# Kernel tuning notes

Measured on AMD Instinct MI355X. Metric: run time of the kernel, lower is better.

## Reference

```python
import jax, jax.numpy as jnp
import numpy as np

H, HKV, D, BS, NSEL, WIN = 32, 8, 64, 64, 16, 512
N_REP = H // HKV


def precompute_freqs(dim, max_seq_len, theta=10000.0):
    inv = 1.0 / theta ** (np.arange(0, dim, 2, dtype=np.float32) / dim)
    t = np.arange(max_seq_len, dtype=np.float32)
    return jnp.asarray(np.outer(t, inv))  # (S, dim//2)


def apply_rope(x, freqs):
    # x: (B, T, H, D)
    T = x.shape[1]
    xr = x.reshape(x.shape[:-1] + (-1, 2))
    cos = jnp.cos(freqs[:T])[None, :, None, :]
    sin = jnp.sin(freqs[:T])[None, :, None, :]
    x0, x1 = xr[..., 0], xr[..., 1]
    out = jnp.stack([x0 * cos - x1 * sin, x0 * sin + x1 * cos], axis=-1)
    return out.reshape(x.shape)


def setup_inputs() -> dict:
    key = jax.random.key(0)
    ks = jax.random.split(key, 9)
    d_model = 2048
    s = lambda fan_in: 1.0 / np.sqrt(fan_in)
    return {
        "x": jax.random.normal(ks[0], (1, 2048, d_model), jnp.float32),
        "W_q": jax.random.normal(ks[1], (d_model, H * D), jnp.float32) * s(d_model),
        "W_k": jax.random.normal(ks[2], (d_model, HKV * D), jnp.float32) * s(d_model),
        "W_v": jax.random.normal(ks[3], (d_model, HKV * D), jnp.float32) * s(d_model),
        "W_o": jax.random.normal(ks[4], (H * D, d_model), jnp.float32) * s(H * D),
        "W_ck": jax.random.normal(ks[5], (BS * D, D), jnp.float32) * s(BS * D),
        "W_cv": jax.random.normal(ks[6], (BS * D, D), jnp.float32) * s(BS * D),
        "W_imp": jax.random.normal(ks[7], (D, 1), jnp.float32) * s(D),
        "W_gate": jax.random.normal(ks[8], (d_model, 3), jnp.float32) * s(d_model),
    }


def reference(x, W_q, W_k, W_v, W_o, W_ck, W_cv, W_imp, W_gate):
    B, T, _ = x.shape
    S = T  # no kv_cache
    scale = 1.0 / np.sqrt(D)
    freqs = precompute_freqs(D, T)

    q = apply_rope((x @ W_q).reshape(B, T, H, D), freqs)
    k = apply_rope((x @ W_k).reshape(B, T, HKV, D), freqs)
    v = (x @ W_v).reshape(B, T, HKV, D)
    q = q.transpose(0, 2, 1, 3)  # (B,H,T,D)
    k = k.transpose(0, 2, 1, 3)  # (B,HKV,S,D)
    v = v.transpose(0, 2, 1, 3)

    # --- compressed-block branch ---
    nb = S // BS
    kb = k[:, :, : nb * BS].reshape(B, HKV, nb, BS * D)
    vb = v[:, :, : nb * BS].reshape(B, HKV, nb, BS * D)
    kc = jnp.repeat(kb @ W_ck, N_REP, axis=1)  # (B,H,nb,D)
    vc = jnp.repeat(vb @ W_cv, N_REP, axis=1)
    a_c = jax.nn.softmax(jnp.einsum('bhtd,bhnd->bhtn', q, kc) * scale, axis=-1)
    out_c = jnp.einsum('bhtn,bhnd->bhtd', a_c, vc)

    # GQA expansion shared by select / sliding branches
    kx = jnp.repeat(k, N_REP, axis=1)
    vx = jnp.repeat(v, N_REP, axis=1)

    # --- 'selected' branch (reference computes top-k indices but discards them;
    # attention is full dense unmasked softmax, faithfully reproduced) ---
    k_mean = k[:, :, : nb * BS].reshape(B, HKV, nb, BS, D).mean(axis=3)
    scores = (k_mean @ W_imp)[..., 0]
    _top = jax.lax.top_k(scores, NSEL)  # dead code in original; kept for faithfulness
    a_s = jax.nn.softmax(jnp.einsum('bhtd,bhsd->bhts', q, kx) * scale, axis=-1)
    out_s = jnp.einsum('bhts,bhsd->bhtd', a_s, vx)

    # --- sliding-window branch (dense scores + mask, as in original) ---
    logits = jnp.einsum('bhtd,bhsd->bhts', q, kx) * scale
    i = jnp.arange(T)[:, None]
    j = jnp.arange(S)[None, :]
    allowed = (j <= S - T + i) & (j >= S - T + i - WIN + 1)
    logits = jnp.where(allowed[None, None], logits, -jnp.inf)
    a_w = jnp.nan_to_num(jax.nn.softmax(logits, axis=-1))
    out_w = jnp.einsum('bhts,bhsd->bhtd', a_w, vx)

    # --- gated combine ---
    gates = jax.nn.softmax(x @ W_gate, axis=-1)  # (B,T,3)
    stacked = jnp.stack(
        [out_c.transpose(0, 2, 1, 3), out_s.transpose(0, 2, 1, 3), out_w.transpose(0, 2, 1, 3)],
        axis=3,
    )  # (B,T,H,3,D)
    out = (stacked * gates[:, :, None, :, None]).sum(axis=3).reshape(B, T, H * D)
    return out @ W_o
```

## Files before the change

kernel.cpp:

```cpp
#include <hip/hip_runtime.h>
#include <cmath>

typedef unsigned short u16;
typedef unsigned int u32;
typedef __attribute__((ext_vector_type(8))) __bf16 bf16x8;
typedef __attribute__((ext_vector_type(8))) u16 u16x8;
typedef __attribute__((ext_vector_type(4))) float f32x4;
typedef __attribute__((ext_vector_type(4))) u16 u16x4;

#define MFMA16(acc, a, b) (acc) = __builtin_amdgcn_mfma_f32_16x16x32_bf16((a), (b), (acc), 0, 0, 0)

__device__ __forceinline__ u16 f2bf(float x) {
  union { float f; u32 u; } c; c.f = x;
  u32 r = (c.u + 0x7FFFu + ((c.u >> 16) & 1u)) >> 16;
  return (u16)r;
}
__device__ __forceinline__ float bf2f(u16 b) {
  union { u32 u; float f; } c; c.u = ((u32)b) << 16;
  return c.f;
}
__device__ __forceinline__ float rowmax16(float v) {
#pragma unroll
  for (int m = 1; m < 16; m <<= 1) v = fmaxf(v, __shfl_xor(v, m));
  return v;
}
__device__ __forceinline__ float rowsum16(float v) {
#pragma unroll
  for (int m = 1; m < 16; m <<= 1) v += __shfl_xor(v, m);
  return v;
}
__device__ __forceinline__ void gload16(const u16* g, u16* l) {
  __builtin_amdgcn_global_load_lds(
      (const __attribute__((address_space(1))) void*)(g),
      (__attribute__((address_space(3))) void*)(l), 16, 0, 0);
}
__device__ __forceinline__ float exp2_asm(float x) {
  float r;
  asm("v_exp_f32 %0, %1\n\ts_nop 0" : "=v"(r) : "v"(x));
  return r;
}
__device__ __forceinline__ u32 cvtpk(float a, float b) {
  u32 r;
  asm("v_cvt_pk_bf16_f32 %0, %1, %2" : "=v"(r) : "v"(a), "v"(b));
  return r;
}
__device__ __forceinline__ u16x8 bc_u(bf16x8 v) { union { bf16x8 b; u16x8 u; } c; c.b = v; return c.u; }
__device__ __forceinline__ bf16x8 bc_b(u16x8 v) { union { u16x8 u; bf16x8 b; } c; c.u = v; return c.b; }
__device__ __forceinline__ bf16x8 pack8(f32x4 a, f32x4 b) {
  union { u32 w[4]; bf16x8 v; } c;
  c.w[0] = cvtpk(a[0], a[1]);
  c.w[1] = cvtpk(a[2], a[3]);
  c.w[2] = cvtpk(b[0], b[1]);
  c.w[3] = cvtpk(b[2], b[3]);
  return c.v;
}

__global__ void freqs_kernel(float* __restrict__ ct, float* __restrict__ st) {
  int idx = blockIdx.x * 256 + threadIdx.x;
  int t = idx >> 5, i = idx & 31;
  float inv = 1.0f / powf(10000.0f, (float)i / 32.0f);
  float a = (float)t * inv;
  float sv, cv;
  sincosf(a, &sv, &cv);
  ct[idx] = cv;
  st[idx] = sv;
}

__global__ void cvt_x_kernel(const float* __restrict__ in, u16* __restrict__ out) {
  int idx = (blockIdx.x * 256 + threadIdx.x) * 4;
  f32x4 v = *(const f32x4*)(in + idx);
  u16x4 o;
  o[0] = f2bf(v[0]); o[1] = f2bf(v[1]); o[2] = f2bf(v[2]); o[3] = f2bf(v[3]);
  *(u16x4*)(out + idx) = o;
}

__global__ __launch_bounds__(256) void trcvt_kernel(const float* __restrict__ W,
                                                    u16* __restrict__ Wt, int K, int N) {
  __shared__ u16 t_lds[64][65];
  int ntx = N >> 6;
  int kt = (blockIdx.x / ntx) * 64, nt = (blockIdx.x % ntx) * 64;
  int tx = threadIdx.x & 63, ty4 = threadIdx.x >> 6;
#pragma unroll 4
  for (int yy = 0; yy < 16; ++yy) {
    int k = kt + ty4 * 16 + yy;
    t_lds[ty4 * 16 + yy][tx] = f2bf(W[(size_t)k * N + nt + tx]);
  }
  __syncthreads();
#pragma unroll 4
  for (int yy = 0; yy < 16; ++yy) {
    int n = nt + ty4 * 16 + yy;
    Wt[(size_t)n * K + kt + tx] = t_lds[tx][ty4 * 16 + yy];
  }
}

__global__ __launch_bounds__(256) void gemm_bt_kernel(const u16* __restrict__ A,
                                                      const u16* __restrict__ Bt,
                                                      float* __restrict__ C,
                                                      int M, int N, int K) {
  __shared__ __align__(16) u16 As[128 * 64];
  __shared__ __align__(16) u16 Bs[128 * 64];
  const int tid = threadIdx.x;
  const int lane = tid & 63;
  const int w = tid >> 6;
  const int lr = lane & 15;
  const int lg = lane >> 4;
  const int lk8 = lg * 8;
  const int gx = gridDim.x;
  const int nwg = gx * gridDim.y;
  const int flat = blockIdx.y * gx + blockIdx.x;
  const int qq = nwg >> 3;
  const int swz = (flat & 7) * qq + (flat >> 3);
  const int brow = (swz % gx) * 128;
  const int bcol = (swz / gx) * 128;
  const int wr = (w >> 1) * 64;
  const int wc = (w & 1) * 64;

  const f32x4 zero4 = {0.f, 0.f, 0.f, 0.f};
  f32x4 acc[4][4];
#pragma unroll
  for (int m = 0; m < 4; ++m)
#pragma unroll
    for (int n = 0; n < 4; ++n) acc[m][n] = zero4;

  const int srow = tid >> 3;
  const int scol = (tid & 7) * 8;
  const u16* Ab = A + (size_t)(brow + srow) * K + scol;
  const u16* Bb = Bt + (size_t)(bcol + srow) * K + scol;

  for (int k0 = 0; k0 < K; k0 += 64) {
    __syncthreads();
#pragma unroll
    for (int it = 0; it < 4; ++it) {
      gload16(Ab + (size_t)it * 32 * K + k0, &As[tid * 8 + it * 2048]);
      gload16(Bb + (size_t)it * 32 * K + k0, &Bs[tid * 8 + it * 2048]);
    }
    __syncthreads();
#pragma unroll
    for (int kk = 0; kk < 2; ++kk) {
      bf16x8 af[4], bv[4];
#pragma unroll
      for (int m = 0; m < 4; ++m)
        af[m] = *(const bf16x8*)&As[(wr + m * 16 + lr) * 64 + kk * 32 + lk8];
#pragma unroll
      for (int n = 0; n < 4; ++n)
        bv[n] = *(const bf16x8*)&Bs[(wc + n * 16 + lr) * 64 + kk * 32 + lk8];
#pragma unroll
      for (int m = 0; m < 4; ++m)
#pragma unroll
        for (int n = 0; n < 4; ++n) MFMA16(acc[m][n], af[m], bv[n]);
    }
  }
#pragma unroll
  for (int m = 0; m < 4; ++m) {
#pragma unroll
    for (int rr = 0; rr < 4; ++rr) {
      int row = brow + wr + m * 16 + lg * 4 + rr;
#pragma unroll
      for (int n = 0; n < 4; ++n)
        C[(size_t)row * N + bcol + wc + n * 16 + lr] = acc[m][n][rr];
    }
  }
}

__global__ void rope_q_kernel(const float* __restrict__ qkv, const float* __restrict__ ct,
                              const float* __restrict__ st, u16* __restrict__ qb) {
  int idx = blockIdx.x * 256 + threadIdx.x;
  int i = idx & 31, hh = (idx >> 5) & 31, t = idx >> 10;
  float x0 = qkv[(size_t)t * 3072 + hh * 64 + 2 * i];
  float x1 = qkv[(size_t)t * 3072 + hh * 64 + 2 * i + 1];
  float c = ct[t * 32 + i], s = st[t * 32 + i];
  size_t o = ((size_t)hh * 2048 + t) * 64 + 2 * i;
  qb[o] = f2bf((x0 * c - x1 * s) * 0.125f);
  qb[o + 1] = f2bf((x0 * s + x1 * c) * 0.125f);
}
__global__ void rope_k_kernel(const float* __restrict__ qkv, const float* __restrict__ ct,
                              const float* __restrict__ st, u16* __restrict__ kb) {
  int idx = blockIdx.x * 256 + threadIdx.x;
  int i = idx & 31, hh = (idx >> 5) & 7, t = idx >> 8;
  float x0 = qkv[(size_t)t * 3072 + 2048 + hh * 64 + 2 * i];
  float x1 = qkv[(size_t)t * 3072 + 2048 + hh * 64 + 2 * i + 1];
  float c = ct[t * 32 + i], s = st[t * 32 + i];
  size_t o = ((size_t)hh * 2048 + t) * 64 + 2 * i;
  kb[o] = f2bf(x0 * c - x1 * s);
  kb[o + 1] = f2bf(x0 * s + x1 * c);
}
__global__ __launch_bounds__(256) void vtrans_kernel(const float* __restrict__ qkv,
                                                     u16* __restrict__ vbr,
                                                     u16* __restrict__ vb2) {
  __shared__ u16 tl[64][72];
  int hk = blockIdx.y, t0 = blockIdx.x * 64;
  int tx = threadIdx.x & 63, ty = threadIdx.x >> 6;
#pragma unroll 4
  for (int yy = 0; yy < 16; ++yy) {
    int row = ty * 16 + yy;
    u16 b = f2bf(qkv[(size_t)(t0 + row) * 3072 + 2560 + hk * 64 + tx]);
    tl[row][tx] = b;
    vbr[((size_t)hk * 2048 + t0 + row) * 64 + tx] = b;
  }
  __syncthreads();
  u16* dst = vb2 + (size_t)hk * 64 * 2048 + t0;
#pragma unroll 4
  for (int yy = 0; yy < 16; ++yy)
    dst[(size_t)(ty * 16 + yy) * 2048 + tx] = tl[tx][ty * 16 + yy];
}

__global__ __launch_bounds__(256) void gates_kernel(const float* __restrict__ x,
                                                    const float* __restrict__ Wg,
                                                    float* __restrict__ g) {
  int t = blockIdx.x * 4 + (threadIdx.x >> 6);
  int lane = threadIdx.x & 63;
  const float* xr = x + (size_t)t * 2048;
  float a0 = 0, a1 = 0, a2 = 0;
  for (int d = lane; d < 2048; d += 64) {
    float xv = xr[d];
    a0 = fmaf(xv, Wg[d * 3 + 0], a0);
    a1 = fmaf(xv, Wg[d * 3 + 1], a1);
    a2 = fmaf(xv, Wg[d * 3 + 2], a2);
  }
#pragma unroll
  for (int msk = 1; msk < 64; msk <<= 1) {
    a0 += __shfl_xor(a0, msk);
    a1 += __shfl_xor(a1, msk);
    a2 += __shfl_xor(a2, msk);
  }
  if (lane == 0) {
    float m = fmaxf(a0, fmaxf(a1, a2));
    float e0 = __expf(a0 - m), e1 = __expf(a1 - m), e2 = __expf(a2 - m);
    float inv = 1.f / (e0 + e1 + e2);
    g[t * 3 + 0] = e0 * inv; g[t * 3 + 1] = e1 * inv; g[t * 3 + 2] = e2 * inv;
  }
}

__global__ __launch_bounds__(256) void cgemm_kernel(const u16* __restrict__ kB,
                                                    const u16* __restrict__ vbr,
                                                    const float* __restrict__ Wck,
                                                    const float* __restrict__ Wcv,
                                                    float* __restrict__ kc,
                                                    float* __restrict__ vc) {
  __shared__ float red[4][64];
  int b = blockIdx.x;
  bool isv = b >= 256;
  int blk = b & 255;
  const u16* src = (isv ? vbr : kB) + (size_t)blk * 4096;
  const float* W = isv ? Wcv : Wck;
  float* out = (isv ? vc : kc) + (size_t)blk * 64;
  int lane = threadIdx.x & 63, w = threadIdx.x >> 6;
  int base = w * 1024;
  float acc0 = 0.f, acc1 = 0.f;
  for (int i = 0; i < 1024; i += 8) {
    u16x8 s8 = *(const u16x8*)(src + base + i);
#pragma unroll
    for (int j = 0; j < 8; j += 2) {
      acc0 = fmaf(bf2f(s8[j]), W[(size_t)(base + i + j) * 64 + lane], acc0);
      acc1 = fmaf(bf2f(s8[j + 1]), W[(size_t)(base + i + j + 1) * 64 + lane], acc1);
    }
  }
  red[w][lane] = acc0 + acc1;
  __syncthreads();
  if (w == 0)
    out[lane] = red[0][lane] + red[1][lane] + red[2][lane] + red[3][lane];
}

__global__ __launch_bounds__(256) void attn_kernel(
    const u16* __restrict__ qb, const u16* __restrict__ kb, const u16* __restrict__ vb2,
    const float* __restrict__ kcf, const float* __restrict__ vcf,
    const float* __restrict__ gf, u16* __restrict__ comb) {
  __shared__ __align__(16) u16 k_lds[2][64 * 64];
  __shared__ __align__(16) u16 vt_lds[2][64 * 64];
  __shared__ __align__(16) u16 p_lds[4][16 * 64];

  const int tid = threadIdx.x;
  const int lane = tid & 63;
  const int w = tid >> 6;
  const int lr = lane & 15;
  const int lg = lane >> 4;
  const int lk8 = lg * 8;
  const int flat = blockIdx.y * gridDim.x + blockIdx.x;
  const int swz = (flat & 7) * 128 + (flat >> 3);
  const int h = swz >> 5;
  const int t0 = (swz & 31) * 64;
  const int hk = h >> 2;
  const int tw = t0 + w * 16;
  const f32x4 zero4 = {0.f, 0.f, 0.f, 0.f};
  const float LOG2E = 1.44269504f;
  const float THR = 11.5416f;

  bf16x8 qf0, qf1;
  {
    const u16* qrow = qb + ((size_t)h * 2048 + (tw + lr)) * 64;
    qf0 = *(const bf16x8*)(qrow + lk8);
    qf1 = *(const bf16x8*)(qrow + 32 + lk8);
  }

  const int lin1 = 256 + tid;
  const int row0 = tid >> 3, sl0 = (tid & 7) ^ (row0 & 7);
  const int row1 = lin1 >> 3, sl1 = (lin1 & 7) ^ (row1 & 7);
  const u16* kS0 = kb + ((size_t)hk * 2048 + row0) * 64 + sl0 * 8;
  const u16* kS1 = kb + ((size_t)hk * 2048 + row1) * 64 + sl1 * 8;
  const u16* vS0 = vb2 + ((size_t)hk * 64 + row0) * 2048 + sl0 * 8;
  const u16* vS1 = vb2 + ((size_t)hk * 64 + row1) * 2048 + sl1 * 8;

  const int sA = ((0 + lg) ^ (lr & 7)) * 8;
  const int sB = ((4 + lg) ^ (lr & 7)) * 8;

  f32x4 acc_s[4], acc_w[4];
#pragma unroll
  for (int n = 0; n < 4; ++n) { acc_s[n] = zero4; acc_w[n] = zero4; }
  float m2[4], lsr[4], lwr[4];
#pragma unroll
  for (int r = 0; r < 4; ++r) { m2[r] = -1e30f; lsr[r] = 0.f; lwr[r] = 0.f; }

#define STAGE(cc)                                                      \
  {                                                                    \
    const int b_ = (cc) & 1;                                           \
    gload16(kS0 + (size_t)(cc) * 4096, &k_lds[b_][tid * 8]);           \
    gload16(kS1 + (size_t)(cc) * 4096, &k_lds[b_][2048 + tid * 8]);    \
    gload16(vS0 + (cc) * 64, &vt_lds[b_][tid * 8]);                    \
    gload16(vS1 + (cc) * 64, &vt_lds[b_][2048 + tid * 8]);             \
  }

  STAGE(0);
  __syncthreads();

#pragma unroll 1
  for (int c = 0; c < 32; ++c) {
    const int s0 = c * 64;
    const u16* kbuf = k_lds[c & 1];
    const u16* vbuf = vt_lds[c & 1];
    if (c < 31) STAGE(c + 1);

    f32x4 sc[4];
    __builtin_amdgcn_s_setprio(1);
#pragma unroll
    for (int cb = 0; cb < 4; ++cb) {
      f32x4 z = zero4;
      const int rb = (cb * 16 + lr) * 64;
      bf16x8 b0 = *(const bf16x8*)&kbuf[rb + sA];
      bf16x8 b1 = *(const bf16x8*)&kbuf[rb + sB];
      MFMA16(z, qf0, b0);
      MFMA16(z, qf1, b1);
      sc[cb] = z;
    }
    __builtin_amdgcn_s_setprio(0);

    const bool winAct = (s0 <= tw + 15) && (s0 + 63 >= tw - 511);
    const int dbase = tw + lg * 4 - s0 - lr;

    float mxl[4];
#pragma unroll
    for (int r = 0; r < 4; ++r)
      mxl[r] = fmaxf(fmaxf(sc[0][r], sc[1][r]), fmaxf(sc[2][r], sc[3][r]));
    float dmax = fmaxf(fmaxf(fmaf(mxl[0], LOG2E, -m2[0]), fmaf(mxl[1], LOG2E, -m2[1])),
                       fmaxf(fmaf(mxl[2], LOG2E, -m2[2]), fmaf(mxl[3], LOG2E, -m2[3])));
    if (__any(dmax > THR)) {
#pragma unroll
      for (int r = 0; r < 4; ++r) {
        float mnew = fmaxf(m2[r], rowmax16(mxl[r]) * LOG2E);
        float corr = exp2_asm(m2[r] - mnew);
        m2[r] = mnew;
        lsr[r] *= corr;
        lwr[r] *= corr;
#pragma unroll
        for (int n = 0; n < 4; ++n) { acc_s[n][r] *= corr; acc_w[n][r] *= corr; }
      }
    }

#pragma unroll
    for (int r = 0; r < 4; ++r) {
      float pv0 = exp2_asm(fmaf(sc[0][r], LOG2E, -m2[r]));
      float pv1 = exp2_asm(fmaf(sc[1][r], LOG2E, -m2[r]));
      float pv2 = exp2_asm(fmaf(sc[2][r], LOG2E, -m2[r]));
      float pv3 = exp2_asm(fmaf(sc[3][r], LOG2E, -m2[r]));
      lsr[r] += (pv0 + pv1) + (pv2 + pv3);
      if (winAct) {
        int d0 = dbase + r;
        float s = 0.f;
        s += ((u32)d0 < 512u) ? pv0 : 0.f;
        s += ((u32)(d0 - 16) < 512u) ? pv1 : 0.f;
        s += ((u32)(d0 - 32) < 512u) ? pv2 : 0.f;
        s += ((u32)(d0 - 48) < 512u) ? pv3 : 0.f;
        lwr[r] += s;
      }
      u32 pk01 = cvtpk(pv0, pv1), pk23 = cvtpk(pv2, pv3);
      const int prow = lg * 4 + r;
      const int pb = prow * 64 + (lr & 7);
      const int rh = prow & 7;
      const int shi = lr >> 3;
      u16* pl = p_lds[w];
      pl[pb + ((0 + shi) ^ rh) * 8] = (u16)pk01;
      pl[pb + ((2 + shi) ^ rh) * 8] = (u16)(pk01 >> 16);
      pl[pb + ((4 + shi) ^ rh) * 8] = (u16)pk23;
      pl[pb + ((6 + shi) ^ rh) * 8] = (u16)(pk23 >> 16);
    }
    asm volatile("s_waitcnt lgkmcnt(0)" ::: "memory");
    bf16x8 ap0 = *(const bf16x8*)&p_lds[w][lr * 64 + sA];
    bf16x8 ap1 = *(const bf16x8*)&p_lds[w][lr * 64 + sB];

    bf16x8 aw0 = ap0, aw1 = ap1;
    if (winAct) {
      const int base0 = (tw + lr) - (s0 + lk8);
      u16x8 a0 = bc_u(ap0), a1 = bc_u(ap1);
      u16x8 z0, z1;
#pragma unroll
      for (int j = 0; j < 8; ++j) {
        z0[j] = ((u32)(base0 - j) < 512u) ? a0[j] : (u16)0;
        z1[j] = ((u32)(base0 - 32 - j) < 512u) ? a1[j] : (u16)0;
      }
      aw0 = bc_b(z0);
      aw1 = bc_b(z1);
    }

    __builtin_amdgcn_s_setprio(1);
#pragma unroll
    for (int n = 0; n < 4; ++n) {
      const int rb = (n * 16 + lr) * 64;
      bf16x8 bv0 = *(const bf16x8*)&vbuf[rb + sA];
      bf16x8 bv1 = *(const bf16x8*)&vbuf[rb + sB];
      MFMA16(acc_s[n], ap0, bv0);
      MFMA16(acc_s[n], ap1, bv1);
      if (winAct) {
        MFMA16(acc_w[n], aw0, bv0);
        MFMA16(acc_w[n], aw1, bv1);
      }
    }
    __builtin_amdgcn_s_setprio(0);

    __syncthreads();
  }
#undef STAGE

  f32x4 accc[4];
  float lcv[4];
  {
    f32x4 sc0 = zero4, sc1 = zero4;
#pragma unroll
    for (int kk = 0; kk < 2; ++kk) {
      const float* kr0 = kcf + ((size_t)hk * 32 + 0 * 16 + lr) * 64 + kk * 32 + lk8;
      const float* kr1 = kcf + ((size_t)hk * 32 + 1 * 16 + lr) * 64 + kk * 32 + lk8;
      bf16x8 b0 = pack8(*(const f32x4*)kr0, *(const f32x4*)(kr0 + 4));
      bf16x8 b1 = pack8(*(const f32x4*)kr1, *(const f32x4*)(kr1 + 4));
      bf16x8 qk = kk ? qf1 : qf0;
      MFMA16(sc0, qk, b0);
      MFMA16(sc1, qk, b1);
    }
#pragma unroll
    for (int r = 0; r < 4; ++r) {
      float a = sc0[r], b = sc1[r];
      float m = rowmax16(fmaxf(a, b));
      float p0 = __expf(a - m), p1 = __expf(b - m);
      lcv[r] = rowsum16(p0 + p1);
      u32 pk = cvtpk(p0, p1);
      const int prow = lg * 4 + r;
      const int pb = prow * 64 + (lr & 7);
      const int rh = prow & 7;
      const int shi = lr >> 3;
      u16* pl = p_lds[w];
      pl[pb + ((0 + shi) ^ rh) * 8] = (u16)pk;
      pl[pb + ((2 + shi) ^ rh) * 8] = (u16)(pk >> 16);
    }
    asm volatile("s_waitcnt lgkmcnt(0)" ::: "memory");
    bf16x8 ap = *(const bf16x8*)&p_lds[w][lr * 64 + sA];
#pragma unroll
    for (int nb = 0; nb < 4; ++nb) {
      u16x8 bb;
#pragma unroll
      for (int j = 0; j < 8; ++j)
        bb[j] = f2bf(vcf[((size_t)hk * 32 + lk8 + j) * 64 + nb * 16 + lr]);
      f32x4 z = zero4;
      MFMA16(z, ap, bc_b(bb));
      accc[nb] = z;
    }
  }

#pragma unroll
  for (int r = 0; r < 4; ++r) {
    float ls = rowsum16(lsr[r]);
    float lw = rowsum16(lwr[r]);
    int t = tw + lg * 4 + r;
    float g0 = gf[t * 3 + 0], g1 = gf[t * 3 + 1], g2 = gf[t * 3 + 2];
    float wc_ = g0 / lcv[r];
    float ws_ = g1 / ls;
    float ww_ = g2 / lw;
#pragma unroll
    for (int n = 0; n < 4; ++n) {
      float val = accc[n][r] * wc_ + acc_s[n][r] * ws_ + acc_w[n][r] * ww_;
      comb[(size_t)t * 2048 + h * 64 + n * 16 + lr] = f2bf(val);
    }
  }
}

extern "C" void kernel_launch(void* const* d_in, const int* in_sizes, int n_in,
                              void* d_out, int out_size, void* d_ws, size_t ws_size,
                              hipStream_t stream) {
  (void)in_sizes; (void)n_in; (void)out_size;
  const float* x   = (const float*)d_in[0];
  const float* Wq  = (const float*)d_in[1];
  const float* Wk  = (const float*)d_in[2];
  const float* Wv  = (const float*)d_in[3];
  const float* Wo  = (const float*)d_in[4];
  const float* Wck = (const float*)d_in[5];
  const float* Wcv = (const float*)d_in[6];
  const float* Wg  = (const float*)d_in[8];
  float* out = (float*)d_out;
  char* ws = (char*)d_ws;

  constexpr size_t OXB   = 0;
  constexpr size_t OWT   = OXB  + 8388608;
  constexpr size_t OWOT  = OWT  + 12582912;
  constexpr size_t OQKV  = OWOT + 8388608;
  constexpr size_t OQB   = OQKV + 25165824;
  constexpr size_t OKB   = OQB  + 8388608;
  constexpr size_t OVB   = OKB  + 2097152;
  constexpr size_t OCT   = OVB  + 2097152;
  constexpr size_t OST   = OCT  + 262144;
  constexpr size_t OKC   = OST  + 262144;
  constexpr size_t OVC   = OKC  + 65536;
  constexpr size_t OG    = OVC  + 65536;
  constexpr size_t OCOMB = OG   + 24576;
  constexpr size_t TOTAL = OCOMB + 8388608;
  if (ws_size < TOTAL) return;

  u16* xb    = (u16*)(ws + OXB);
  u16* WT    = (u16*)(ws + OWT);
  u16* WoT   = (u16*)(ws + OWOT);
  float* qkv = (float*)(ws + OQKV);
  u16* qB    = (u16*)(ws + OQB);
  u16* kB    = (u16*)(ws + OKB);
  u16* vB2   = (u16*)(ws + OVB);
  float* ct  = (float*)(ws + OCT);
  float* st  = (float*)(ws + OST);
  float* kc  = (float*)(ws + OKC);
  float* vc  = (float*)(ws + OVC);
  float* gg  = (float*)(ws + OG);
  u16* comb  = (u16*)(ws + OCOMB);
  u16* vbr   = comb;

  freqs_kernel<<<dim3(256), dim3(256), 0, stream>>>(ct, st);
  cvt_x_kernel<<<dim3(4096), dim3(256), 0, stream>>>(x, xb);
  trcvt_kernel<<<dim3(1024), dim3(256), 0, stream>>>(Wq, WT, 2048, 2048);
  trcvt_kernel<<<dim3(256),  dim3(256), 0, stream>>>(Wk, WT + (size_t)2048 * 2048, 2048, 512);
  trcvt_kernel<<<dim3(256),  dim3(256), 0, stream>>>(Wv, WT + (size_t)2560 * 2048, 2048, 512);
  trcvt_kernel<<<dim3(1024), dim3(256), 0, stream>>>(Wo, WoT, 2048, 2048);

  gemm_bt_kernel<<<dim3(16, 24), dim3(256), 0, stream>>>(xb, WT, qkv, 2048, 3072, 2048);

  rope_q_kernel<<<dim3(8192), dim3(256), 0, stream>>>(qkv, ct, st, qB);
  rope_k_kernel<<<dim3(2048), dim3(256), 0, stream>>>(qkv, ct, st, kB);
  vtrans_kernel<<<dim3(32, 8), dim3(256), 0, stream>>>(qkv, vbr, vB2);
  gates_kernel<<<dim3(512), dim3(256), 0, stream>>>(x, Wg, gg);

  cgemm_kernel<<<dim3(512), dim3(256), 0, stream>>>(kB, vbr, Wck, Wcv, kc, vc);

  attn_kernel<<<dim3(32, 32), dim3(256), 0, stream>>>(qB, kB, vB2, kc, vc, gg, comb);

  gemm_bt_kernel<<<dim3(16, 16), dim3(256), 0, stream>>>(comb, WoT, out, 2048, 2048, 2048);
}
```

Baseline: 278.8 us.

## Transpose MFMA operands and build P fragments in registers via permlane swaps

Swaps the A/B operands of the QK^T and PV MFMAs so each lane owns one query row. Row max and row sum then need only two cross-lane shuffles instead of a 16-lane reduction per row, and the online-softmax state becomes a scalar per lane. The P fragment for the PV MFMA is assembled with v_permlane32/16_swap instructions instead of a round trip through shared memory with a waitcnt, and the per-wave P buffer is removed. Output stores become vectorized 4-element writes. The permlane-based repacking must exactly match the MFMA operand layout, so there is some correctness risk.

```diff
diff --git a/kernel.cpp b/kernel.cpp
--- a/kernel.cpp
+++ b/kernel.cpp
@@ -53,6 +53,10 @@
   c.w[2] = cvtpk(b[0], b[1]);
   c.w[3] = cvtpk(b[2], b[3]);
   return c.v;
+}
+__device__ __forceinline__ void swapchain(u32& a, u32& c) {
+  asm("v_permlane32_swap_b32 %0, %1" : "+v"(a), "+v"(c));
+  asm("v_permlane16_swap_b32 %0, %1" : "+v"(a), "+v"(c));
 }
 
 __global__ void freqs_kernel(float* __restrict__ ct, float* __restrict__ st) {
@@ -267,14 +271,13 @@
     const float* __restrict__ gf, u16* __restrict__ comb) {
   __shared__ __align__(16) u16 k_lds[2][64 * 64];
   __shared__ __align__(16) u16 vt_lds[2][64 * 64];
-  __shared__ __align__(16) u16 p_lds[4][16 * 64];
 
   const int tid = threadIdx.x;
   const int lane = tid & 63;
-  const int w = tid >> 6;
   const int lr = lane & 15;
   const int lg = lane >> 4;
   const int lk8 = lg * 8;
+  const int w = tid >> 6;
   const int flat = blockIdx.y * gridDim.x + blockIdx.x;
   const int swz = (flat & 7) * 128 + (flat >> 3);
   const int h = swz >> 5;
@@ -306,9 +309,7 @@
   f32x4 acc_s[4], acc_w[4];
 #pragma unroll
   for (int n = 0; n < 4; ++n) { acc_s[n] = zero4; acc_w[n] = zero4; }
-  float m2[4], lsr[4], lwr[4];
-#pragma unroll
-  for (int r = 0; r < 4; ++r) { m2[r] = -1e30f; lsr[r] = 0.f; lwr[r] = 0.f; }
+  float m2 = -1e30f, lsr = 0.f, lwr = 0.f;
 
 #define STAGE(cc)                                                      \
   {                                                                    \
@@ -337,69 +338,68 @@
       const int rb = (cb * 16 + lr) * 64;
       bf16x8 b0 = *(const bf16x8*)&kbuf[rb + sA];
       bf16x8 b1 = *(const bf16x8*)&kbuf[rb + sB];
-      MFMA16(z, qf0, b0);
-      MFMA16(z, qf1, b1);
+      MFMA16(z, b0, qf0);
+      MFMA16(z, b1, qf1);
       sc[cb] = z;
     }
     __builtin_amdgcn_s_setprio(0);
 
     const bool winAct = (s0 <= tw + 15) && (s0 + 63 >= tw - 511);
-    const int dbase = tw + lg * 4 - s0 - lr;
-
-    float mxl[4];
-#pragma unroll
-    for (int r = 0; r < 4; ++r)
-      mxl[r] = fmaxf(fmaxf(sc[0][r], sc[1][r]), fmaxf(sc[2][r], sc[3][r]));
-    float dmax = fmaxf(fmaxf(fmaf(mxl[0], LOG2E, -m2[0]), fmaf(mxl[1], LOG2E, -m2[1])),
-                       fmaxf(fmaf(mxl[2], LOG2E, -m2[2]), fmaf(mxl[3], LOG2E, -m2[3])));
-    if (__any(dmax > THR)) {
+
+    float mxl = -1e30f;
+#pragma unroll
+    for (int cb = 0; cb < 4; ++cb)
+#pragma unroll
+      for (int r = 0; r < 4; ++r) mxl = fmaxf(mxl, sc[cb][r]);
+    if (__any(fmaf(mxl, LOG2E, -m2) > THR)) {
+      float gm = mxl;
+      gm = fmaxf(gm, __shfl_xor(gm, 16));
+      gm = fmaxf(gm, __shfl_xor(gm, 32));
+      float mnew = fmaxf(m2, gm * LOG2E);
+      float corr = exp2_asm(m2 - mnew);
+      m2 = mnew;
+      lsr *= corr;
+      lwr *= corr;
+#pragma unroll
+      for (int n = 0; n < 4; ++n) { acc_s[n] *= corr; acc_w[n] *= corr; }
+    }
+
+    float pv[4][4];
+#pragma unroll
+    for (int cb = 0; cb < 4; ++cb)
 #pragma unroll
       for (int r = 0; r < 4; ++r) {
-        float mnew = fmaxf(m2[r], rowmax16(mxl[r]) * LOG2E);
-        float corr = exp2_asm(m2[r] - mnew);
-        m2[r] = mnew;
-        lsr[r] *= corr;
-        lwr[r] *= corr;
-#pragma unroll
-        for (int n = 0; n < 4; ++n) { acc_s[n][r] *= corr; acc_w[n][r] *= corr; }
+        pv[cb][r] = exp2_asm(fmaf(sc[cb][r], LOG2E, -m2));
+        lsr += pv[cb][r];
       }
-    }
-
-#pragma unroll
-    for (int r = 0; r < 4; ++r) {
-      float pv0 = exp2_asm(fmaf(sc[0][r], LOG2E, -m2[r]));
-      float pv1 = exp2_asm(fmaf(sc[1][r], LOG2E, -m2[r]));
-      float pv2 = exp2_asm(fmaf(sc[2][r], LOG2E, -m2[r]));
-      float pv3 = exp2_asm(fmaf(sc[3][r], LOG2E, -m2[r]));
-      lsr[r] += (pv0 + pv1) + (pv2 + pv3);
-      if (winAct) {
-        int d0 = dbase + r;
-        float s = 0.f;
-        s += ((u32)d0 < 512u) ? pv0 : 0.f;
-        s += ((u32)(d0 - 16) < 512u) ? pv1 : 0.f;
-        s += ((u32)(d0 - 32) < 512u) ? pv2 : 0.f;
-        s += ((u32)(d0 - 48) < 512u) ? pv3 : 0.f;
-        lwr[r] += s;
-      }
-      u32 pk01 = cvtpk(pv0, pv1), pk23 = cvtpk(pv2, pv3);
-      const int prow = lg * 4 + r;
-      const int pb = prow * 64 + (lr & 7);
-      const int rh = prow & 7;
-      const int shi = lr >> 3;
-      u16* pl = p_lds[w];
-      pl[pb + ((0 + shi) ^ rh) * 8] = (u16)pk01;
-      pl[pb + ((2 + shi) ^ rh) * 8] = (u16)(pk01 >> 16);
-      pl[pb + ((4 + shi) ^ rh) * 8] = (u16)pk23;
-      pl[pb + ((6 + shi) ^ rh) * 8] = (u16)(pk23 >> 16);
-    }
-    asm volatile("s_waitcnt lgkmcnt(0)" ::: "memory");
-    bf16x8 ap0 = *(const bf16x8*)&p_lds[w][lr * 64 + sA];
-    bf16x8 ap1 = *(const bf16x8*)&p_lds[w][lr * 64 + sB];
-
-    bf16x8 aw0 = ap0, aw1 = ap1;
+    if (winAct) {
+      const int dbase2 = (tw + lr) - s0 - lg * 4;
+#pragma unroll
+      for (int cb = 0; cb < 4; ++cb)
+#pragma unroll
+        for (int r = 0; r < 4; ++r) {
+          int d0 = dbase2 - 16 * cb - r;
+          lwr += ((u32)d0 < 512u) ? pv[cb][r] : 0.f;
+        }
+    }
+
+    u32 A0 = cvtpk(pv[0][0], pv[0][1]), B0 = cvtpk(pv[0][2], pv[0][3]);
+    u32 C0 = cvtpk(pv[1][0], pv[1][1]), D0 = cvtpk(pv[1][2], pv[1][3]);
+    u32 A1 = cvtpk(pv[2][0], pv[2][1]), B1 = cvtpk(pv[2][2], pv[2][3]);
+    u32 C1 = cvtpk(pv[3][0], pv[3][1]), D1 = cvtpk(pv[3][2], pv[3][3]);
+    swapchain(A0, C0);
+    swapchain(B0, D0);
+    swapchain(A1, C1);
+    swapchain(B1, D1);
+    union { u32 wd[4]; bf16x8 v; } pf0c, pf1c;
+    pf0c.wd[0] = A0; pf0c.wd[1] = B0; pf0c.wd[2] = C0; pf0c.wd[3] = D0;
+    pf1c.wd[0] = A1; pf1c.wd[1] = B1; pf1c.wd[2] = C1; pf1c.wd[3] = D1;
+    bf16x8 pf0 = pf0c.v, pf1 = pf1c.v;
+
+    bf16x8 aw0 = pf0, aw1 = pf1;
     if (winAct) {
       const int base0 = (tw + lr) - (s0 + lk8);
-      u16x8 a0 = bc_u(ap0), a1 = bc_u(ap1);
+      u16x8 a0 = bc_u(pf0), a1 = bc_u(pf1);
       u16x8 z0, z1;
 #pragma unroll
       for (int j = 0; j < 8; ++j) {
@@ -416,11 +416,11 @@
       const int rb = (n * 16 + lr) * 64;
       bf16x8 bv0 = *(const bf16x8*)&vbuf[rb + sA];
       bf16x8 bv1 = *(const bf16x8*)&vbuf[rb + sB];
-      MFMA16(acc_s[n], ap0, bv0);
-      MFMA16(acc_s[n], ap1, bv1);
+      MFMA16(acc_s[n], bv0, pf0);
+      MFMA16(acc_s[n], bv1, pf1);
       if (winAct) {
-        MFMA16(acc_w[n], aw0, bv0);
-        MFMA16(acc_w[n], aw1, bv1);
+        MFMA16(acc_w[n], bv0, aw0);
+        MFMA16(acc_w[n], bv1, aw1);
       }
     }
     __builtin_amdgcn_s_setprio(0);
@@ -430,36 +430,41 @@
 #undef STAGE
 
   f32x4 accc[4];
-  float lcv[4];
+  float lcv;
   {
     f32x4 sc0 = zero4, sc1 = zero4;
 #pragma unroll
     for (int kk = 0; kk < 2; ++kk) {
-      const float* kr0 = kcf + ((size_t)hk * 32 + 0 * 16 + lr) * 64 + kk * 32 + lk8;
-      const float* kr1 = kcf + ((size_t)hk * 32 + 1 * 16 + lr) * 64 + kk * 32 + lk8;
+      const float* kr0 = kcf + ((size_t)hk * 32 + lr) * 64 + kk * 32 + lk8;
+      const float* kr1 = kcf + ((size_t)hk * 32 + 16 + lr) * 64 + kk * 32 + lk8;
       bf16x8 b0 = pack8(*(const f32x4*)kr0, *(const f32x4*)(kr0 + 4));
       bf16x8 b1 = pack8(*(const f32x4*)kr1, *(const f32x4*)(kr1 + 4));
       bf16x8 qk = kk ? qf1 : qf0;
-      MFMA16(sc0, qk, b0);
-      MFMA16(sc1, qk, b1);
-    }
+      MFMA16(sc0, b0, qk);
+      MFMA16(sc1, b1, qk);
+    }
+    float mm = -1e30f;
+#pragma unroll
+    for (int r = 0; r < 4; ++r) mm = fmaxf(mm, fmaxf(sc0[r], sc1[r]));
+    mm = fmaxf(mm, __shfl_xor(mm, 16));
+    mm = fmaxf(mm, __shfl_xor(mm, 32));
+    float p0[4], p1[4];
+    float ssum = 0.f;
 #pragma unroll
     for (int r = 0; r < 4; ++r) {
-      float a = sc0[r], b = sc1[r];
-      float m = rowmax16(fmaxf(a, b));
-      float p0 = __expf(a - m), p1 = __expf(b - m);
-      lcv[r] = rowsum16(p0 + p1);
-      u32 pk = cvtpk(p0, p1);
-      const int prow = lg * 4 + r;
-      const int pb = prow * 64 + (lr & 7);
-      const int rh = prow & 7;
-      const int shi = lr >> 3;
-      u16* pl = p_lds[w];
-      pl[pb + ((0 + shi) ^ rh) * 8] = (u16)pk;
-      pl[pb + ((2 + shi) ^ rh) * 8] = (u16)(pk >> 16);
-    }
-    asm volatile("s_waitcnt lgkmcnt(0)" ::: "memory");
-    bf16x8 ap = *(const bf16x8*)&p_lds[w][lr * 64 + sA];
+      p0[r] = __expf(sc0[r] - mm);
+      p1[r] = __expf(sc1[r] - mm);
+      ssum += p0[r] + p1[r];
+    }
+    ssum += __shfl_xor(ssum, 16);
+    ssum += __shfl_xor(ssum, 32);
+    lcv = ssum;
+    u32 A = cvtpk(p0[0], p0[1]), B = cvtpk(p0[2], p0[3]);
+    u32 C = cvtpk(p1[0], p1[1]), D = cvtpk(p1[2], p1[3]);
+    swapchain(A, C);
+    swapchain(B, D);
+    union { u32 wd[4]; bf16x8 v; } pc;
+    pc.wd[0] = A; pc.wd[1] = B; pc.wd[2] = C; pc.wd[3] = D;
 #pragma unroll
     for (int nb = 0; nb < 4; ++nb) {
       u16x8 bb;
@@ -467,24 +472,30 @@
       for (int j = 0; j < 8; ++j)
         bb[j] = f2bf(vcf[((size_t)hk * 32 + lk8 + j) * 64 + nb * 16 + lr]);
       f32x4 z = zero4;
-      MFMA16(z, ap, bc_b(bb));
+      MFMA16(z, bc_b(bb), pc.v);
       accc[nb] = z;
     }
   }
 
-#pragma unroll
-  for (int r = 0; r < 4; ++r) {
-    float ls = rowsum16(lsr[r]);
-    float lw = rowsum16(lwr[r]);
-    int t = tw + lg * 4 + r;
+  float ls = lsr;
+  ls += __shfl_xor(ls, 16);
+  ls += __shfl_xor(ls, 32);
+  float lw = lwr;
+  lw += __shfl_xor(lw, 16);
+  lw += __shfl_xor(lw, 32);
+  {
+    const int t = tw + lr;
     float g0 = gf[t * 3 + 0], g1 = gf[t * 3 + 1], g2 = gf[t * 3 + 2];
-    float wc_ = g0 / lcv[r];
+    float wc_ = g0 / lcv;
     float ws_ = g1 / ls;
     float ww_ = g2 / lw;
 #pragma unroll
     for (int n = 0; n < 4; ++n) {
-      float val = accc[n][r] * wc_ + acc_s[n][r] * ws_ + acc_w[n][r] * ww_;
-      comb[(size_t)t * 2048 + h * 64 + n * 16 + lr] = f2bf(val);
+      u16x4 o;
+#pragma unroll
+      for (int r = 0; r < 4; ++r)
+        o[r] = f2bf(accc[n][r] * wc_ + acc_s[n][r] * ws_ + acc_w[n][r] * ww_);
+      *(u16x4*)&comb[(size_t)t * 2048 + h * 64 + n * 16 + lg * 4] = o;
     }
   }
 }
```

Result: faster. 269.3 us (-3.4%).
